# Optimization experiments

Hardware: AMD Instinct MI355X
Metric: run time of the kernel (lower is better)

The kernel has to match this reference:

```python
import jax, jax.numpy as jnp
import numpy as np

N_NODES = 50000
N_EDGES = 800000
NDIM_IN = 64
EDIMS = 64
NDIM_OUT = 128


def setup_inputs() -> dict:
    key = jax.random.key(0)
    k = jax.random.split(key, 8)
    nfeats = jax.random.normal(k[0], (N_NODES, NDIM_IN), dtype=jnp.float32)
    efeats = jax.random.normal(k[1], (N_EDGES, EDIMS), dtype=jnp.float32)
    # Linear weights stored as [in, out]; scaled for stable activations.
    W_msg = jax.random.normal(k[2], (NDIM_IN + EDIMS, NDIM_OUT), dtype=jnp.float32) * 0.05
    b_msg = jax.random.normal(k[3], (NDIM_OUT,), dtype=jnp.float32) * 0.05
    W_apply = jax.random.normal(k[4], (NDIM_IN + NDIM_OUT, NDIM_OUT), dtype=jnp.float32) * 0.05
    b_apply = jax.random.normal(k[5], (NDIM_OUT,), dtype=jnp.float32) * 0.05
    src = jax.random.randint(k[6], (N_EDGES,), 0, N_NODES, dtype=jnp.int64)
    dst = jax.random.randint(k[7], (N_EDGES,), 0, N_NODES, dtype=jnp.int64)
    return {
        "nfeats": nfeats,
        "efeats": efeats,
        "W_msg": W_msg,
        "b_msg": b_msg,
        "W_apply": W_apply,
        "b_apply": b_apply,
        "src": src,
        "dst": dst,
    }


def reference(nfeats, efeats, W_msg, b_msg, W_apply, b_apply, src, dst):
    # message: per-edge gather src node feats, concat with edge feats, linear+relu
    msg_in = jnp.concatenate([nfeats[src], efeats], axis=1)          # [E, ndim_in+edims]
    m = jax.nn.relu(msg_in @ W_msg + b_msg)                           # [E, ndim_out]
    # aggregate: sum messages into destination nodes
    h_neigh = jax.ops.segment_sum(m, dst, num_segments=nfeats.shape[0])  # [N, ndim_out]
    # update: concat original node feats with aggregated messages, linear+relu
    out = jax.nn.relu(jnp.concatenate([nfeats, h_neigh], axis=1) @ W_apply + b_apply)
    return out
```

## Files before the change

kernel.cpp:

```cpp
#include <hip/hip_runtime.h>
#include <hip/hip_bf16.h>

#define N_NODES  50000
#define N_EDGES  800000
#define NDIM_IN  64
#define EDIMS    64
#define NDIM_OUT 128

typedef __bf16 bf16;
typedef bf16  bf16x8 __attribute__((ext_vector_type(8)));
typedef float f32x4  __attribute__((ext_vector_type(4)));

__device__ __forceinline__ bool detect_f32(const void* nfeats) {
    const unsigned short* w = (const unsigned short*)nfeats;
    for (int i = 0; i < 64; i += 2) {
        const int e = (w[i] >> 7) & 0xFF;
        if (e < 100 || e > 134) return true;
    }
    return false;
}
__device__ __forceinline__ bool detect_i64(const int* p) {
    for (int i = 1; i < 64; i += 2) if (p[i] != 0) return false;
    return true;
}

__device__ __forceinline__ bf16x8 load8(const void* p, int off, bool f32) {
    if (f32) {
        const float* q = (const float*)p + off;
        const f32x4 a = *(const f32x4*)q;
        const f32x4 b = *(const f32x4*)(q + 4);
        bf16x8 r;
        #pragma unroll
        for (int u = 0; u < 4; ++u) { r[u] = (bf16)a[u]; r[4 + u] = (bf16)b[u]; }
        return r;
    }
    return *(const bf16x8*)((const bf16*)p + off);
}
__device__ __forceinline__ float loadf(const void* p, int i, bool f32) {
    return f32 ? ((const float*)p)[i] : (float)((const bf16*)p)[i];
}
__device__ __forceinline__ void storef(void* p, int i, float v, bool f32) {
    if (f32) ((float*)p)[i] = v; else ((bf16*)p)[i] = (bf16)v;
}

__global__ __launch_bounds__(256) void hist_kernel(const int* __restrict__ dst,
                                                   int* __restrict__ cnt) {
    __shared__ int s_ish;
    if (threadIdx.x == 0) s_ish = detect_i64(dst) ? 1 : 0;
    __syncthreads();
    const int ish = s_ish;
    const int stride = gridDim.x * blockDim.x;
    for (int e = blockIdx.x * blockDim.x + threadIdx.x; e < N_EDGES; e += stride)
        atomicAdd(&cnt[dst[e << ish]], 1);
}

__global__ __launch_bounds__(1024) void scan_kernel(int* __restrict__ cnt,
                                                    int* __restrict__ row_ptr) {
    __shared__ int sp[1024];
    const int t = threadIdx.x;
    const int PER = 49;
    const int base = t * PER;
    int s = 0;
    for (int j = 0; j < PER; ++j) {
        const int i = base + j;
        if (i < N_NODES) s += cnt[i];
    }
    sp[t] = s;
    __syncthreads();
    for (int off = 1; off < 1024; off <<= 1) {
        const int v = (t >= off) ? sp[t - off] : 0;
        __syncthreads();
        sp[t] += v;
        __syncthreads();
    }
    int run = sp[t] - s;
    for (int j = 0; j < PER; ++j) {
        const int i = base + j;
        if (i < N_NODES) {
            const int c = cnt[i];
            row_ptr[i] = run;
            cnt[i] = run;
            run += c;
        }
    }
    if (t == 0) row_ptr[N_NODES] = N_EDGES;
}

__global__ __launch_bounds__(256) void scatter_kernel(const int* __restrict__ src,
                                                      const int* __restrict__ dst,
                                                      int* __restrict__ cursor,
                                                      int* __restrict__ eid,
                                                      int* __restrict__ srcs) {
    __shared__ int s_ish;
    if (threadIdx.x == 0) s_ish = detect_i64(dst) ? 1 : 0;
    __syncthreads();
    const int ish = s_ish;
    const int stride = gridDim.x * blockDim.x;
    for (int e = blockIdx.x * blockDim.x + threadIdx.x; e < N_EDGES; e += stride) {
        const int d = dst[e << ish];
        const int pos = atomicAdd(&cursor[d], 1);
        eid[pos]  = e;
        srcs[pos] = src[e << ish];
    }
}

__global__ __launch_bounds__(256) void msg_agg_kernel(
    const void* __restrict__ nfeats,
    const void* __restrict__ efeats,
    const void* __restrict__ W_msg,
    const void* __restrict__ b_msg,
    const int*  __restrict__ row_ptr,
    const int*  __restrict__ eid,
    const int*  __restrict__ srcs,
    float*      __restrict__ h_neigh)
{
    __shared__ bf16 sWT[128 * 136];
    __shared__ int s_flags;

    const int tid = threadIdx.x;
    if (tid == 0) s_flags = detect_f32(nfeats) ? 1 : 0;
    __syncthreads();
    const bool f32 = (s_flags & 1) != 0;

    #pragma unroll
    for (int it = 0; it < 8; ++it) {
        const int task = it * 256 + tid;
        const int k = task >> 4;
        const int c = task & 15;
        const bf16x8 w = load8(W_msg, k * 128 + c * 8, f32);
        #pragma unroll
        for (int u = 0; u < 8; ++u) sWT[(c * 8 + u) * 136 + k] = w[u];
    }
    __syncthreads();

    const int wave = tid >> 6;
    const int lane = tid & 63;
    const int m    = lane & 15;
    const int quad = lane >> 4;

    float bias[8];
    #pragma unroll
    for (int t = 0; t < 8; ++t) bias[t] = loadf(b_msg, t * 16 + m, f32);

    const int wstride = gridDim.x * 4;
    for (int v = blockIdx.x * 4 + wave; v < N_NODES; v += wstride) {
        const int beg = row_ptr[v];
        const int deg = row_ptr[v + 1] - beg;

        float hacc[8] = {0.f, 0.f, 0.f, 0.f, 0.f, 0.f, 0.f, 0.f};

        for (int T = 0; T * 16 < deg; ++T) {
            const int r0 = T * 16;
            const int sl = (r0 + m < deg) ? (beg + r0 + m) : beg;
            const int s  = srcs[sl];
            const int e  = eid[sl];

            bf16x8 a[4];
            a[0] = load8(nfeats, s * 64 +      quad * 8, f32);
            a[1] = load8(nfeats, s * 64 + 32 + quad * 8, f32);
            a[2] = load8(efeats, e * 64 +      quad * 8, f32);
            a[3] = load8(efeats, e * 64 + 32 + quad * 8, f32);

            #pragma unroll
            for (int t = 0; t < 8; ++t) {
                f32x4 acc = {0.f, 0.f, 0.f, 0.f};
                const bf16* bp = sWT + (t * 16 + m) * 136 + quad * 8;
                #pragma unroll
                for (int kb = 0; kb < 4; ++kb)
                    acc = __builtin_amdgcn_mfma_f32_16x16x32_bf16(
                              a[kb], *(const bf16x8*)(bp + kb * 32), acc, 0, 0, 0);
                float part = 0.f;
                #pragma unroll
                for (int i = 0; i < 4; ++i) {
                    float val = acc[i] + bias[t];
                    val = val > 0.f ? val : 0.f;
                    if (r0 + quad * 4 + i < deg) part += val;
                }
                hacc[t] += part;
            }
        }

        #pragma unroll
        for (int t = 0; t < 8; ++t) {
            float s = hacc[t];
            s += __shfl_xor(s, 16, 64);
            s += __shfl_xor(s, 32, 64);
            hacc[t] = s;
        }

        const float lo = quad < 2 ? (quad == 0 ? hacc[0] : hacc[1])
                                  : (quad == 2 ? hacc[2] : hacc[3]);
        const float hi = quad < 2 ? (quad == 0 ? hacc[4] : hacc[5])
                                  : (quad == 2 ? hacc[6] : hacc[7]);
        h_neigh[v * 128 + lane]      = lo;
        h_neigh[v * 128 + 64 + lane] = hi;
    }
}

__global__ __launch_bounds__(256) void edge_msg_kernel(
    const void* __restrict__ nfeats,
    const void* __restrict__ efeats,
    const void* __restrict__ W_msg,
    const void* __restrict__ b_msg,
    const int*  __restrict__ src,
    const int*  __restrict__ dst,
    float*      __restrict__ h_neigh)
{
    __shared__ bf16 sWT[128 * 136];
    __shared__ int s_flags;

    const int tid = threadIdx.x;
    if (tid == 0)
        s_flags = (detect_f32(nfeats) ? 1 : 0) | (detect_i64(dst) ? 2 : 0);
    __syncthreads();
    const bool f32 = (s_flags & 1) != 0;
    const int  ish = (s_flags & 2) ? 1 : 0;

    #pragma unroll
    for (int it = 0; it < 8; ++it) {
        const int task = it * 256 + tid;
        const int k = task >> 4;
        const int c = task & 15;
        const bf16x8 w = load8(W_msg, k * 128 + c * 8, f32);
        #pragma unroll
        for (int u = 0; u < 8; ++u) sWT[(c * 8 + u) * 136 + k] = w[u];
    }
    __syncthreads();

    const int wave = tid >> 6;
    const int lane = tid & 63;
    const int m    = lane & 15;
    const int quad = lane >> 4;

    const int nchunks = N_EDGES / 64;
    for (int chunk = blockIdx.x; chunk < nchunks; chunk += gridDim.x) {
        const int ebase = chunk * 64 + wave * 16;
        const int e_m   = ebase + m;
        const int s     = src[e_m << ish];

        bf16x8 a[4];
        a[0] = load8(nfeats, s   * 64 +      quad * 8, f32);
        a[1] = load8(nfeats, s   * 64 + 32 + quad * 8, f32);
        a[2] = load8(efeats, e_m * 64 +      quad * 8, f32);
        a[3] = load8(efeats, e_m * 64 + 32 + quad * 8, f32);

        int drow[4];
        #pragma unroll
        for (int i = 0; i < 4; ++i)
            drow[i] = dst[(ebase + quad * 4 + i) << ish] * 128;

        #pragma unroll
        for (int t = 0; t < 8; ++t) {
            f32x4 acc = {0.f, 0.f, 0.f, 0.f};
            const bf16* bp = sWT + (t * 16 + m) * 136 + quad * 8;
            #pragma unroll
            for (int kb = 0; kb < 4; ++kb)
                acc = __builtin_amdgcn_mfma_f32_16x16x32_bf16(
                          a[kb], *(const bf16x8*)(bp + kb * 32), acc, 0, 0, 0);
            const int   n    = t * 16 + m;
            const float bias = loadf(b_msg, n, f32);
            #pragma unroll
            for (int i = 0; i < 4; ++i) {
                float v = acc[i] + bias;
                v = v > 0.f ? v : 0.f;
                unsafeAtomicAdd(h_neigh + drow[i] + n, v);
            }
        }
    }
}

__global__ __launch_bounds__(256) void apply_kernel(
    const void*  __restrict__ nfeats,
    const float* __restrict__ h_neigh,
    const void*  __restrict__ W_apply,
    const void*  __restrict__ b_apply,
    void*        __restrict__ out)
{
    __shared__ bf16 sWT[128 * 200];
    __shared__ int s_flags;

    const int tid = threadIdx.x;
    if (tid == 0) s_flags = detect_f32(nfeats) ? 1 : 0;
    __syncthreads();
    const bool f32 = (s_flags & 1) != 0;

    #pragma unroll
    for (int it = 0; it < 12; ++it) {
        const int task = it * 256 + tid;
        const int k = task >> 4;
        const int c = task & 15;
        const bf16x8 w = load8(W_apply, k * 128 + c * 8, f32);
        #pragma unroll
        for (int u = 0; u < 8; ++u) sWT[(c * 8 + u) * 200 + k] = w[u];
    }
    __syncthreads();

    const int wave = tid >> 6;
    const int lane = tid & 63;
    const int m    = lane & 15;
    const int quad = lane >> 4;

    const int nchunks = (N_NODES + 63) / 64;
    for (int chunk = blockIdx.x; chunk < nchunks; chunk += gridDim.x) {
        const int nbase = chunk * 64 + wave * 16;
        const int nm  = nbase + m;
        const int nmc = nm < N_NODES ? nm : N_NODES - 1;

        bf16x8 a[6];
        a[0] = load8(nfeats, nmc * 64 +      quad * 8, f32);
        a[1] = load8(nfeats, nmc * 64 + 32 + quad * 8, f32);
        #pragma unroll
        for (int kb = 0; kb < 4; ++kb) {
            const float* hp = h_neigh + nmc * 128 + kb * 32 + quad * 8;
            const f32x4 p = *(const f32x4*)(hp);
            const f32x4 q = *(const f32x4*)(hp + 4);
            bf16x8 r;
            #pragma unroll
            for (int u = 0; u < 4; ++u) { r[u] = (bf16)p[u]; r[4 + u] = (bf16)q[u]; }
            a[2 + kb] = r;
        }

        #pragma unroll
        for (int t = 0; t < 8; ++t) {
            f32x4 acc = {0.f, 0.f, 0.f, 0.f};
            const bf16* bp = sWT + (t * 16 + m) * 200 + quad * 8;
            #pragma unroll
            for (int kb = 0; kb < 6; ++kb)
                acc = __builtin_amdgcn_mfma_f32_16x16x32_bf16(
                          a[kb], *(const bf16x8*)(bp + kb * 32), acc, 0, 0, 0);
            const int   n    = t * 16 + m;
            const float bias = loadf(b_apply, n, f32);
            #pragma unroll
            for (int i = 0; i < 4; ++i) {
                const int row = nbase + quad * 4 + i;
                if (row < N_NODES) {
                    float v = acc[i] + bias;
                    v = v > 0.f ? v : 0.f;
                    storef(out, row * 128 + n, v, f32);
                }
            }
        }
    }
}

extern "C" void kernel_launch(void* const* d_in, const int* in_sizes, int n_in,
                              void* d_out, int out_size, void* d_ws, size_t ws_size,
                              hipStream_t stream) {
    const void* nfeats  = d_in[0];
    const void* efeats  = d_in[1];
    const void* W_msg   = d_in[2];
    const void* b_msg   = d_in[3];
    const void* W_apply = d_in[4];
    const void* b_apply = d_in[5];
    const int*  src     = (const int*)d_in[6];
    const int*  dst     = (const int*)d_in[7];

    float* h_neigh = (float*)d_ws;

    const size_t OFF_ROWPTR = 25600000;
    const size_t OFF_CNT    = OFF_ROWPTR + 200064;
    const size_t OFF_EID    = OFF_CNT + 200064;
    const size_t OFF_SRCS   = OFF_EID + 3200000;
    const size_t NEED       = OFF_SRCS + 3200000;

    if (ws_size >= NEED) {
        int* row_ptr = (int*)((char*)d_ws + OFF_ROWPTR);
        int* cnt     = (int*)((char*)d_ws + OFF_CNT);
        int* eid     = (int*)((char*)d_ws + OFF_EID);
        int* srcs    = (int*)((char*)d_ws + OFF_SRCS);

        hipMemsetAsync(cnt, 0, (size_t)N_NODES * sizeof(int), stream);
        hist_kernel<<<1024, 256, 0, stream>>>(dst, cnt);
        scan_kernel<<<1, 1024, 0, stream>>>(cnt, row_ptr);
        scatter_kernel<<<1024, 256, 0, stream>>>(src, dst, cnt, eid, srcs);
        msg_agg_kernel<<<1024, 256, 0, stream>>>(nfeats, efeats, W_msg, b_msg,
                                                 row_ptr, eid, srcs, h_neigh);
    } else {
        hipMemsetAsync(h_neigh, 0, (size_t)N_NODES * NDIM_OUT * sizeof(float), stream);
        edge_msg_kernel<<<768, 256, 0, stream>>>(nfeats, efeats, W_msg, b_msg,
                                                 src, dst, h_neigh);
    }

    apply_kernel<<<512, 256, 0, stream>>>(nfeats, h_neigh, W_apply, b_apply, d_out);
}
```

Baseline: 680.9 us.

## Pre-gather edge inputs into dst-sorted dense bf16 buffer before message GEMM

Adds a gather kernel that places each edge's source-node and edge features, converted to bf16, into a dense buffer in destination-sorted order while doing the CSR scatter. The message/aggregate kernel then reads contiguous rows instead of doing indirect gathers. The scan is rewritten with vectorized int4 loads and wave shuffles, and the apply grid grows. This costs an extra write and read of a 200MB buffer in exchange for removing the random gathers from the MFMA kernel, and it needs a larger workspace.

```diff
diff --git a/kernel.cpp b/kernel.cpp
--- a/kernel.cpp
+++ b/kernel.cpp
@@ -24,7 +24,7 @@
     return true;
 }
 
-__device__ __forceinline__ bf16x8 load8(const void* p, int off, bool f32) {
+__device__ __forceinline__ bf16x8 load8(const void* p, long off, bool f32) {
     if (f32) {
         const float* q = (const float*)p + off;
         const f32x4 a = *(const f32x4*)q;
@@ -56,62 +56,98 @@
 
 __global__ __launch_bounds__(1024) void scan_kernel(int* __restrict__ cnt,
                                                     int* __restrict__ row_ptr) {
-    __shared__ int sp[1024];
-    const int t = threadIdx.x;
-    const int PER = 49;
-    const int base = t * PER;
-    int s = 0;
-    for (int j = 0; j < PER; ++j) {
-        const int i = base + j;
-        if (i < N_NODES) s += cnt[i];
-    }
-    sp[t] = s;
-    __syncthreads();
-    for (int off = 1; off < 1024; off <<= 1) {
-        const int v = (t >= off) ? sp[t - off] : 0;
-        __syncthreads();
-        sp[t] += v;
-        __syncthreads();
-    }
-    int run = sp[t] - s;
-    for (int j = 0; j < PER; ++j) {
-        const int i = base + j;
-        if (i < N_NODES) {
-            const int c = cnt[i];
-            row_ptr[i] = run;
-            cnt[i] = run;
-            run += c;
-        }
-    }
-    if (t == 0) row_ptr[N_NODES] = N_EDGES;
-}
-
-__global__ __launch_bounds__(256) void scatter_kernel(const int* __restrict__ src,
-                                                      const int* __restrict__ dst,
-                                                      int* __restrict__ cursor,
-                                                      int* __restrict__ eid,
-                                                      int* __restrict__ srcs) {
-    __shared__ int s_ish;
-    if (threadIdx.x == 0) s_ish = detect_i64(dst) ? 1 : 0;
-    __syncthreads();
-    const int ish = s_ish;
-    const int stride = gridDim.x * blockDim.x;
-    for (int e = blockIdx.x * blockDim.x + threadIdx.x; e < N_EDGES; e += stride) {
-        const int d = dst[e << ish];
-        const int pos = atomicAdd(&cursor[d], 1);
-        eid[pos]  = e;
-        srcs[pos] = src[e << ish];
-    }
-}
-
-__global__ __launch_bounds__(256) void msg_agg_kernel(
+    __shared__ int sw[16];
+    const int t    = threadIdx.x;
+    const int lane = t & 63;
+    const int w    = t >> 6;
+    const int base = t * 52;
+
+    int sum = 0;
+    #pragma unroll
+    for (int j = 0; j < 13; ++j) {
+        const int4 q = *(const int4*)(cnt + base + j * 4);
+        sum += q.x + q.y + q.z + q.w;
+    }
+    int s = sum;
+    #pragma unroll
+    for (int off = 1; off < 64; off <<= 1) {
+        const int u = __shfl_up(s, off, 64);
+        if (lane >= off) s += u;
+    }
+    if (lane == 63) sw[w] = s;
+    __syncthreads();
+    if (t < 16) {
+        int x = sw[t];
+        #pragma unroll
+        for (int off = 1; off < 16; off <<= 1) {
+            const int u = __shfl_up(x, off, 16);
+            if ((t & 15) >= off) x += u;
+        }
+        sw[t] = x;
+    }
+    __syncthreads();
+    int run = (w > 0 ? sw[w - 1] : 0) + (s - sum);
+    #pragma unroll
+    for (int j = 0; j < 13; ++j) {
+        const int4 q = *(const int4*)(cnt + base + j * 4);
+        int4 r;
+        r.x = run; run += q.x;
+        r.y = run; run += q.y;
+        r.z = run; run += q.z;
+        r.w = run; run += q.w;
+        *(int4*)(row_ptr + base + j * 4) = r;
+        *(int4*)(cnt     + base + j * 4) = r;
+    }
+}
+
+__global__ __launch_bounds__(256) void gather_kernel(
     const void* __restrict__ nfeats,
     const void* __restrict__ efeats,
+    const int*  __restrict__ src,
+    const int*  __restrict__ dst,
+    int*        __restrict__ cursor,
+    bf16*       __restrict__ A)
+{
+    __shared__ int s_flags;
+    const int tid = threadIdx.x;
+    if (tid == 0)
+        s_flags = (detect_f32(nfeats) ? 1 : 0) | (detect_i64(dst) ? 2 : 0);
+    __syncthreads();
+    const bool f32 = (s_flags & 1) != 0;
+    const int  ish = (s_flags & 2) ? 1 : 0;
+
+    const int lane = tid & 63;
+    const int wave = tid >> 6;
+    const int c    = lane & 3;
+    const int ei   = lane >> 2;
+
+    const int ngroups = N_EDGES / 16;
+    const int nw      = gridDim.x * 4;
+    for (int g = blockIdx.x * 4 + wave; g < ngroups; g += nw) {
+        const int e = g * 16 + ei;
+        int pos = 0;
+        if (c == 0) pos = atomicAdd(&cursor[dst[(long)e << ish]], 1);
+        pos = __shfl(pos, lane & ~3, 64);
+        const int s_ = src[(long)e << ish];
+
+        const void* bsrc = (c < 2) ? nfeats : efeats;
+        const int   row  = (c < 2) ? s_ : e;
+        const int   ko   = (c & 1) * 32;
+        bf16* outp = A + (size_t)pos * 128 + c * 32;
+        #pragma unroll
+        for (int j = 0; j < 4; ++j) {
+            const bf16x8 v = load8(bsrc, (long)row * 64 + ko + j * 8, f32);
+            *(bf16x8*)(outp + j * 8) = v;
+        }
+    }
+}
+
+__global__ __launch_bounds__(256) void msg_agg_dense(
+    const void* __restrict__ nfeats,
+    const bf16* __restrict__ A,
     const void* __restrict__ W_msg,
     const void* __restrict__ b_msg,
     const int*  __restrict__ row_ptr,
-    const int*  __restrict__ eid,
-    const int*  __restrict__ srcs,
     float*      __restrict__ h_neigh)
 {
     __shared__ bf16 sWT[128 * 136];
@@ -152,14 +188,12 @@
         for (int T = 0; T * 16 < deg; ++T) {
             const int r0 = T * 16;
             const int sl = (r0 + m < deg) ? (beg + r0 + m) : beg;
-            const int s  = srcs[sl];
-            const int e  = eid[sl];
+            const bf16* ap = A + (size_t)sl * 128 + quad * 8;
 
             bf16x8 a[4];
-            a[0] = load8(nfeats, s * 64 +      quad * 8, f32);
-            a[1] = load8(nfeats, s * 64 + 32 + quad * 8, f32);
-            a[2] = load8(efeats, e * 64 +      quad * 8, f32);
-            a[3] = load8(efeats, e * 64 + 32 + quad * 8, f32);
+            #pragma unroll
+            for (int kb = 0; kb < 4; ++kb)
+                a[kb] = *(const bf16x8*)(ap + kb * 32);
 
             #pragma unroll
             for (int t = 0; t < 8; ++t) {
@@ -197,6 +231,117 @@
     }
 }
 
+__global__ __launch_bounds__(256) void scatter_kernel(const int* __restrict__ src,
+                                                      const int* __restrict__ dst,
+                                                      int* __restrict__ cursor,
+                                                      int* __restrict__ eid,
+                                                      int* __restrict__ srcs) {
+    __shared__ int s_ish;
+    if (threadIdx.x == 0) s_ish = detect_i64(dst) ? 1 : 0;
+    __syncthreads();
+    const int ish = s_ish;
+    const int stride = gridDim.x * blockDim.x;
+    for (int e = blockIdx.x * blockDim.x + threadIdx.x; e < N_EDGES; e += stride) {
+        const int d = dst[(long)e << ish];
+        const int pos = atomicAdd(&cursor[d], 1);
+        eid[pos]  = e;
+        srcs[pos] = src[(long)e << ish];
+    }
+}
+
+__global__ __launch_bounds__(256) void msg_agg_kernel(
+    const void* __restrict__ nfeats,
+    const void* __restrict__ efeats,
+    const void* __restrict__ W_msg,
+    const void* __restrict__ b_msg,
+    const int*  __restrict__ row_ptr,
+    const int*  __restrict__ eid,
+    const int*  __restrict__ srcs,
+    float*      __restrict__ h_neigh)
+{
+    __shared__ bf16 sWT[128 * 136];
+    __shared__ int s_flags;
+
+    const int tid = threadIdx.x;
+    if (tid == 0) s_flags = detect_f32(nfeats) ? 1 : 0;
+    __syncthreads();
+    const bool f32 = (s_flags & 1) != 0;
+
+    #pragma unroll
+    for (int it = 0; it < 8; ++it) {
+        const int task = it * 256 + tid;
+        const int k = task >> 4;
+        const int c = task & 15;
+        const bf16x8 w = load8(W_msg, k * 128 + c * 8, f32);
+        #pragma unroll
+        for (int u = 0; u < 8; ++u) sWT[(c * 8 + u) * 136 + k] = w[u];
+    }
+    __syncthreads();
+
+    const int wave = tid >> 6;
+    const int lane = tid & 63;
+    const int m    = lane & 15;
+    const int quad = lane >> 4;
+
+    float bias[8];
+    #pragma unroll
+    for (int t = 0; t < 8; ++t) bias[t] = loadf(b_msg, t * 16 + m, f32);
+
+    const int wstride = gridDim.x * 4;
+    for (int v = blockIdx.x * 4 + wave; v < N_NODES; v += wstride) {
+        const int beg = row_ptr[v];
+        const int deg = row_ptr[v + 1] - beg;
+
+        float hacc[8] = {0.f, 0.f, 0.f, 0.f, 0.f, 0.f, 0.f, 0.f};
+
+        for (int T = 0; T * 16 < deg; ++T) {
+            const int r0 = T * 16;
+            const int sl = (r0 + m < deg) ? (beg + r0 + m) : beg;
+            const int s  = srcs[sl];
+            const int e  = eid[sl];
+
+            bf16x8 a[4];
+            a[0] = load8(nfeats, (long)s * 64 +      quad * 8, f32);
+            a[1] = load8(nfeats, (long)s * 64 + 32 + quad * 8, f32);
+            a[2] = load8(efeats, (long)e * 64 +      quad * 8, f32);
+            a[3] = load8(efeats, (long)e * 64 + 32 + quad * 8, f32);
+
+            #pragma unroll
+            for (int t = 0; t < 8; ++t) {
+                f32x4 acc = {0.f, 0.f, 0.f, 0.f};
+                const bf16* bp = sWT + (t * 16 + m) * 136 + quad * 8;
+                #pragma unroll
+                for (int kb = 0; kb < 4; ++kb)
+                    acc = __builtin_amdgcn_mfma_f32_16x16x32_bf16(
+                              a[kb], *(const bf16x8*)(bp + kb * 32), acc, 0, 0, 0);
+                float part = 0.f;
+                #pragma unroll
+                for (int i = 0; i < 4; ++i) {
+                    float val = acc[i] + bias[t];
+                    val = val > 0.f ? val : 0.f;
+                    if (r0 + quad * 4 + i < deg) part += val;
+                }
+                hacc[t] += part;
+            }
+        }
+
+        #pragma unroll
+        for (int t = 0; t < 8; ++t) {
+            float s = hacc[t];
+            s += __shfl_xor(s, 16, 64);
+            s += __shfl_xor(s, 32, 64);
+            hacc[t] = s;
+        }
+
+        const float lo = quad < 2 ? (quad == 0 ? hacc[0] : hacc[1])
+                                  : (quad == 2 ? hacc[2] : hacc[3]);
+        const float hi = quad < 2 ? (quad == 0 ? hacc[4] : hacc[5])
+                                  : (quad == 2 ? hacc[6] : hacc[7]);
+        h_neigh[v * 128 + lane]      = lo;
+        h_neigh[v * 128 + 64 + lane] = hi;
+    }
+}
+
 __global__ __launch_bounds__(256) void edge_msg_kernel(
     const void* __restrict__ nfeats,
     const void* __restrict__ efeats,
@@ -236,18 +381,18 @@
     for (int chunk = blockIdx.x; chunk < nchunks; chunk += gridDim.x) {
         const int ebase = chunk * 64 + wave * 16;
         const int e_m   = ebase + m;
-        const int s     = src[e_m << ish];
+        const int s     = src[(long)e_m << ish];
 
         bf16x8 a[4];
-        a[0] = load8(nfeats, s   * 64 +      quad * 8, f32);
-        a[1] = load8(nfeats, s   * 64 + 32 + quad * 8, f32);
-        a[2] = load8(efeats, e_m * 64 +      quad * 8, f32);
-        a[3] = load8(efeats, e_m * 64 + 32 + quad * 8, f32);
+        a[0] = load8(nfeats, (long)s   * 64 +      quad * 8, f32);
+        a[1] = load8(nfeats, (long)s   * 64 + 32 + quad * 8, f32);
+        a[2] = load8(efeats, (long)e_m * 64 +      quad * 8, f32);
+        a[3] = load8(efeats, (long)e_m * 64 + 32 + quad * 8, f32);
 
         int drow[4];
         #pragma unroll
         for (int i = 0; i < 4; ++i)
-            drow[i] = dst[(ebase + quad * 4 + i) << ish] * 128;
+            drow[i] = dst[(long)(ebase + quad * 4 + i) << ish] * 128;
 
         #pragma unroll
         for (int t = 0; t < 8; ++t) {
@@ -307,11 +452,11 @@
         const int nmc = nm < N_NODES ? nm : N_NODES - 1;
 
         bf16x8 a[6];
-        a[0] = load8(nfeats, nmc * 64 +      quad * 8, f32);
-        a[1] = load8(nfeats, nmc * 64 + 32 + quad * 8, f32);
+        a[0] = load8(nfeats, (long)nmc * 64 +      quad * 8, f32);
+        a[1] = load8(nfeats, (long)nmc * 64 + 32 + quad * 8, f32);
         #pragma unroll
         for (int kb = 0; kb < 4; ++kb) {
-            const float* hp = h_neigh + nmc * 128 + kb * 32 + quad * 8;
+            const float* hp = h_neigh + (size_t)nmc * 128 + kb * 32 + quad * 8;
             const f32x4 p = *(const f32x4*)(hp);
             const f32x4 q = *(const f32x4*)(hp + 4);
             bf16x8 r;
@@ -357,19 +502,30 @@
 
     float* h_neigh = (float*)d_ws;
 
+    const size_t SZ_PAD     = 213248;
     const size_t OFF_ROWPTR = 25600000;
-    const size_t OFF_CNT    = OFF_ROWPTR + 200064;
-    const size_t OFF_EID    = OFF_CNT + 200064;
+    const size_t OFF_CNT    = OFF_ROWPTR + SZ_PAD;
+    const size_t OFF_A      = OFF_CNT + SZ_PAD;
+    const size_t NEED_DENSE = OFF_A + (size_t)N_EDGES * 128 * 2;
+    const size_t OFF_EID    = OFF_A;
     const size_t OFF_SRCS   = OFF_EID + 3200000;
-    const size_t NEED       = OFF_SRCS + 3200000;
-
-    if (ws_size >= NEED) {
-        int* row_ptr = (int*)((char*)d_ws + OFF_ROWPTR);
-        int* cnt     = (int*)((char*)d_ws + OFF_CNT);
-        int* eid     = (int*)((char*)d_ws + OFF_EID);
-        int* srcs    = (int*)((char*)d_ws + OFF_SRCS);
-
-        hipMemsetAsync(cnt, 0, (size_t)N_NODES * sizeof(int), stream);
+    const size_t NEED_CSR   = OFF_SRCS + 3200000;
+
+    int* row_ptr = (int*)((char*)d_ws + OFF_ROWPTR);
+    int* cnt     = (int*)((char*)d_ws + OFF_CNT);
+
+    if (ws_size >= NEED_DENSE) {
+        bf16* A = (bf16*)((char*)d_ws + OFF_A);
+        hipMemsetAsync(cnt, 0, (size_t)53248 * sizeof(int), stream);
+        hist_kernel<<<1024, 256, 0, stream>>>(dst, cnt);
+        scan_kernel<<<1, 1024, 0, stream>>>(cnt, row_ptr);
+        gather_kernel<<<1024, 256, 0, stream>>>(nfeats, efeats, src, dst, cnt, A);
+        msg_agg_dense<<<1024, 256, 0, stream>>>(nfeats, A, W_msg, b_msg,
+                                                row_ptr, h_neigh);
+    } else if (ws_size >= NEED_CSR) {
+        int* eid  = (int*)((char*)d_ws + OFF_EID);
+        int* srcs = (int*)((char*)d_ws + OFF_SRCS);
+        hipMemsetAsync(cnt, 0, (size_t)53248 * sizeof(int), stream);
         hist_kernel<<<1024, 256, 0, stream>>>(dst, cnt);
         scan_kernel<<<1, 1024, 0, stream>>>(cnt, row_ptr);
         scatter_kernel<<<1024, 256, 0, stream>>>(src, dst, cnt, eid, srcs);
@@ -381,5 +537,5 @@
                                                  src, dst, h_neigh);
     }
 
-    apply_kernel<<<512, 256, 0, stream>>>(nfeats, h_neigh, W_apply, b_apply, d_out);
-}
+    apply_kernel<<<782, 256, 0, stream>>>(nfeats, h_neigh, W_apply, b_apply, d_out);
+}
```

After: 691.8 us. Within noise of the previous version (+1.6%).
